# Kernel optimization log

Measured on AMD Instinct MI355X. Metric: run time of the kernel, lower is better.

Reference implementation:

```python
import jax, jax.numpy as jnp
import numpy as np

D_MODEL = 1024
NUM_HEADS = 8
D_HEAD = D_MODEL // NUM_HEADS
EPS = 1e-5


def layer_norm(x, gamma, beta):
    mu = jnp.mean(x, axis=-1, keepdims=True)
    var = jnp.mean((x - mu) ** 2, axis=-1, keepdims=True)
    return (x - mu) * jax.lax.rsqrt(var + EPS) * gamma + beta


def setup_inputs() -> dict:
    key = jax.random.key(0)
    ks = jax.random.split(key, 16)
    B, N, M, D = 4, 1024, 1024, D_MODEL
    s = 0.02
    inp = {
        "input_states": jax.random.normal(ks[0], (B, N, D), jnp.float32),
        "memory_states": jax.random.normal(ks[1], (B, M, D), jnp.float32),
        "memory_weights": jax.random.uniform(ks[2], (B, M), jnp.float32),
        "memory_masks": jax.random.randint(ks[3], (B, M), 0, 2).astype(bool),
        "attention_factors": jax.random.uniform(ks[4], (B, N, M), jnp.float32),
        "attention_masks": jax.random.randint(ks[5], (B, 1, N, M), 0, 2).astype(bool),
        "Wq": jax.random.normal(ks[6], (D, D), jnp.float32) * s,
        "bq": jnp.zeros((D,), jnp.float32),
        "Wk": jax.random.normal(ks[7], (D, D), jnp.float32) * s,
        "bk": jnp.zeros((D,), jnp.float32),
        "Wv": jax.random.normal(ks[8], (D, D), jnp.float32) * s,
        "bv": jnp.zeros((D,), jnp.float32),
        "Wo": jax.random.normal(ks[9], (D, D), jnp.float32) * s,
        "bo": jnp.zeros((D,), jnp.float32),
        "g1": jnp.ones((D,), jnp.float32),
        "b1": jnp.zeros((D,), jnp.float32),
        "We": jax.random.normal(ks[10], (2 * D, D), jnp.float32) * s,
        "be": jnp.zeros((2 * D,), jnp.float32),
        "Ws": jax.random.normal(ks[11], (D, 2 * D), jnp.float32) * s,
        "bs": jnp.zeros((D,), jnp.float32),
        "g2": jnp.ones((D,), jnp.float32),
        "b2": jnp.zeros((D,), jnp.float32),
    }
    return inp


def reference(input_states, memory_states, memory_weights, memory_masks,
              attention_factors, attention_masks,
              Wq, bq, Wk, bk, Wv, bv, Wo, bo, g1, b1,
              We, be, Ws, bs, g2, b2):
    B, N, D = input_states.shape
    M = memory_states.shape[1]
    H, C = NUM_HEADS, D_HEAD
    # QKV projections, split heads: (B, H, len, C)
    q = (input_states @ Wq.T + bq).reshape(B, N, H, C).transpose(0, 2, 1, 3)
    k = (memory_states @ Wk.T + bk).reshape(B, M, H, C).transpose(0, 2, 1, 3)
    v = (memory_states @ Wv.T + bv).reshape(B, M, H, C).transpose(0, 2, 1, 3)
    scores = jnp.einsum('bhnc,bhmc->bhnm', q, k) / jnp.sqrt(jnp.float32(C))
    scores = attention_factors[:, None, :, :] * scores
    scores = scores * memory_weights[:, None, None, :]
    neg_inf = jnp.float32(-jnp.inf)
    scores = jnp.where(memory_masks[:, None, None, :], neg_inf, scores)
    scores = jnp.where(attention_masks, neg_inf, scores)
    attn = jax.nn.softmax(scores, axis=-1)  # (B,H,N,M)
    hidden = jnp.einsum('bhnm,bhmc->bhnc', attn, v)
    hidden = hidden.transpose(0, 2, 1, 3).reshape(B, N, D)
    hidden = hidden @ Wo.T + bo
    out1 = layer_norm(hidden + input_states, g1, b1)
    # FFN: expand -> ReLU -> squeeze -> residual + LN
    h = jax.nn.relu(out1 @ We.T + be)
    h = h @ Ws.T + bs
    out = layer_norm(out1 + h, g2, b2)
    return out, attn
```

## Files before the change

### kernel.cpp

```cpp
#include <hip/hip_runtime.h>
#include <hip/hip_bf16.h>

typedef __bf16 bf16_t;
typedef __bf16 bf16x4 __attribute__((ext_vector_type(4)));
typedef __bf16 bf16x8 __attribute__((ext_vector_type(8)));
typedef float f32x4 __attribute__((ext_vector_type(4)));

typedef const __attribute__((address_space(1))) void gvoid_t;
typedef __attribute__((address_space(3))) void lvoid_t;

#define MB (1UL<<20)
#define NEGINF (-__builtin_inff())
#define SCALE 0.08838834764831845f

__device__ __forceinline__ void gload_lds16(const void* g, void* l) {
    __builtin_amdgcn_global_load_lds((gvoid_t*)g, (lvoid_t*)l, 16, 0, 0);
}

__global__ __launch_bounds__(256) void cast_kernel(const float* __restrict__ in,
                                                   bf16_t* __restrict__ out, int n4) {
    int i = blockIdx.x * 256 + threadIdx.x;
    if (i < n4) {
        float4 f = ((const float4*)in)[i];
        bf16x4 o;
        o[0] = (bf16_t)f.x; o[1] = (bf16_t)f.y; o[2] = (bf16_t)f.z; o[3] = (bf16_t)f.w;
        ((bf16x4*)out)[i] = o;
    }
}

template<int TM, int OUT_BF16, int HAS_BIAS, int RELU, int HAS_RES, int VT_OUT>
__global__ __launch_bounds__(256)
void gemm_bt(const bf16_t* __restrict__ Ap, int lda,
             const bf16_t* __restrict__ Bp, int ldb,
             const float* __restrict__ bias,
             const float* __restrict__ res, int ldres,
             void* __restrict__ Cp, int ldc,
             int K, int tilesN,
             long aOffB, long aOffH, long bOffB, long bOffH, long cOffZ, int nH)
{
    __shared__ bf16_t sA[2 * TM * 32];
    __shared__ bf16_t sB[2 * 128 * 32];

    const int z = blockIdx.y;
    const int zb = z / nH, zh = z % nH;
    Ap += zb * aOffB + zh * aOffH;
    Bp += zb * bOffB + zh * bOffH;
    const long cOff = (long)z * cOffZ;

    const int tile = blockIdx.x;
    const int tm = tile / tilesN, tn = tile % tilesN;
    const int rowBase = tm * TM, colBase = tn * 128;
    const int t = threadIdx.x;
    const int wave = t >> 6, lane = t & 63;
    const int wr = (TM == 128) ? ((wave >> 1) * 64) : 0;
    const int wc = (TM == 128) ? ((wave & 1) * 64) : (wave * 32);
    constexpr int NF = (TM == 128) ? 4 : 2;

    f32x4 acc[4][NF] = {};

    const int e0 = t * 8;
    const int srow = e0 >> 5, scol = e0 & 31;

    auto stage = [&](int tt, int bi) {
        const int k0 = tt * 32;
        #pragma unroll
        for (int r = 0; r < TM / 64; ++r) {
            const int row = r * 64 + srow;
            gload_lds16(Ap + (long)(rowBase + row) * lda + k0 + scol,
                        (char*)sA + bi * (TM * 64) + r * 4096 + wave * 1024);
        }
        #pragma unroll
        for (int r = 0; r < 2; ++r) {
            const int row = r * 64 + srow;
            gload_lds16(Bp + (long)(colBase + row) * ldb + k0 + scol,
                        (char*)sB + bi * 8192 + r * 4096 + wave * 1024);
        }
    };

    const int nt = K >> 5;
    stage(0, 0);
    asm volatile("s_waitcnt vmcnt(0)" ::: "memory");
    __syncthreads();

    const int kf = (lane >> 4) * 8;
    const int lr = lane & 15;

    for (int tt = 0; tt < nt; ++tt) {
        const int cur = tt & 1;
        if (tt + 1 < nt) stage(tt + 1, cur ^ 1);

        bf16x8 af[4], bfr[NF];
        #pragma unroll
        for (int m = 0; m < 4; ++m)
            af[m] = *(const bf16x8*)&sA[cur * (TM * 32) + (wr + m * 16 + lr) * 32 + kf];
        #pragma unroll
        for (int n = 0; n < NF; ++n)
            bfr[n] = *(const bf16x8*)&sB[cur * 4096 + (wc + n * 16 + lr) * 32 + kf];
        #pragma unroll
        for (int m = 0; m < 4; ++m)
            #pragma unroll
            for (int n = 0; n < NF; ++n)
                acc[m][n] = __builtin_amdgcn_mfma_f32_16x16x32_bf16(af[m], bfr[n], acc[m][n], 0, 0, 0);

        asm volatile("s_waitcnt vmcnt(0)" ::: "memory");
        __syncthreads();
    }

    #pragma unroll
    for (int m = 0; m < 4; ++m) {
        #pragma unroll
        for (int r = 0; r < 4; ++r) {
            const int i = rowBase + wr + m * 16 + (lane >> 4) * 4 + r;
            #pragma unroll
            for (int n = 0; n < NF; ++n) {
                const int j = colBase + wc + n * 16 + (lane & 15);
                float v = acc[m][n][r];
                if constexpr (HAS_BIAS) v += bias[j];
                if constexpr (RELU) v = fmaxf(v, 0.0f);
                if constexpr (HAS_RES) v += res[(long)i * ldres + j];
                if constexpr (VT_OUT) {
                    const long o = (((long)(i >> 10) * 8 + (j >> 7)) * 128 + (j & 127)) * 1024 + (i & 1023);
                    ((bf16_t*)Cp)[o] = (bf16_t)v;
                } else if constexpr (OUT_BF16) {
                    ((bf16_t*)Cp)[cOff + (long)i * ldc + j] = (bf16_t)v;
                } else {
                    ((float*)Cp)[cOff + (long)i * ldc + j] = v;
                }
            }
        }
    }
}

__global__ __launch_bounds__(256)
void gate_stats_kernel(float* __restrict__ Sio,
                       const float* __restrict__ factors,
                       const float* __restrict__ weights,
                       const int* __restrict__ mmask,
                       const int* __restrict__ amask,
                       float2* __restrict__ stats)
{
    const int row = blockIdx.x * 4 + (threadIdx.x >> 6);
    const int lane = threadIdx.x & 63;
    const int n = row & 1023;
    const int b = row >> 13;
    float4* p = (float4*)(Sio + (long)row * 1024);
    const float4* fac = (const float4*)(factors + ((long)b * 1024 + n) * 1024);
    const float4* wt  = (const float4*)(weights + (long)b * 1024);
    const int4*   mm  = (const int4*)(mmask + (long)b * 1024);
    const int4*   am  = (const int4*)(amask + ((long)b * 1024 + n) * 1024);

    float vals[16];
    float mx = NEGINF;
    #pragma unroll
    for (int jj = 0; jj < 4; ++jj) {
        const int v4 = lane + jj * 64;
        float4 sc = p[v4];
        float4 fa = fac[v4];
        float4 w4 = wt[v4];
        int4 m4 = mm[v4];
        int4 a4 = am[v4];
        float4 g;
        g.x = (m4.x | a4.x) ? NEGINF : sc.x * SCALE * fa.x * w4.x;
        g.y = (m4.y | a4.y) ? NEGINF : sc.y * SCALE * fa.y * w4.y;
        g.z = (m4.z | a4.z) ? NEGINF : sc.z * SCALE * fa.z * w4.z;
        g.w = (m4.w | a4.w) ? NEGINF : sc.w * SCALE * fa.w * w4.w;
        p[v4] = g;
        vals[jj * 4 + 0] = g.x; vals[jj * 4 + 1] = g.y;
        vals[jj * 4 + 2] = g.z; vals[jj * 4 + 3] = g.w;
        mx = fmaxf(mx, fmaxf(fmaxf(g.x, g.y), fmaxf(g.z, g.w)));
    }
    #pragma unroll
    for (int off = 32; off > 0; off >>= 1) mx = fmaxf(mx, __shfl_xor(mx, off));
    float sum = 0.f;
    #pragma unroll
    for (int q = 0; q < 16; ++q) sum += __expf(vals[q] - mx);
    #pragma unroll
    for (int off = 32; off > 0; off >>= 1) sum += __shfl_xor(sum, off);
    if (lane == 0) {
        float2 o; o.x = mx; o.y = 1.0f / sum;
        stats[row] = o;
    }
}

__global__ __launch_bounds__(256)
void pv_kernel(float* __restrict__ Sio,
               const bf16_t* __restrict__ Vtb,
               const float2* __restrict__ stats,
               bf16_t* __restrict__ hidb)
{
    __shared__ bf16_t sA[2 * 64 * 32];
    __shared__ bf16_t sB[2 * 128 * 32];

    const int bh = blockIdx.y;
    const int b = bh >> 3, h = bh & 7;
    const int rowBase = blockIdx.x * 64;
    const int t = threadIdx.x;
    const int wave = t >> 6, lane = t & 63;
    const int wc = wave * 32;

    float* Sp = Sio + (long)bh * 1048576;
    const bf16_t* Bp = Vtb + (long)bh * 131072;

    const int arow = rowBase + (t >> 2);
    const int acol = (t & 3) * 8;
    float* Srow = Sp + (long)arow * 1024 + acol;
    const float2 ML = stats[(long)bh * 1024 + arow];

    f32x4 acc[4][2] = {};

    auto stageB = [&](int tt, int bi) {
        const int k0 = tt * 32;
        #pragma unroll
        for (int r = 0; r < 2; ++r) {
            const int row = r * 64 + ((t * 8) >> 5);
            gload_lds16(Bp + (long)row * 1024 + k0 + ((t * 8) & 31),
                        (char*)sB + bi * 8192 + r * 4096 + wave * 1024);
        }
    };

    auto procA = [&](int tt, int bi, float4 s0, float4 s1) {
        float p[8];
        p[0] = __expf(s0.x - ML.x) * ML.y; p[1] = __expf(s0.y - ML.x) * ML.y;
        p[2] = __expf(s0.z - ML.x) * ML.y; p[3] = __expf(s0.w - ML.x) * ML.y;
        p[4] = __expf(s1.x - ML.x) * ML.y; p[5] = __expf(s1.y - ML.x) * ML.y;
        p[6] = __expf(s1.z - ML.x) * ML.y; p[7] = __expf(s1.w - ML.x) * ML.y;
        float* sp = Srow + tt * 32;
        float4 o0, o1;
        o0.x = p[0]; o0.y = p[1]; o0.z = p[2]; o0.w = p[3];
        o1.x = p[4]; o1.y = p[5]; o1.z = p[6]; o1.w = p[7];
        *(float4*)sp = o0;
        *(float4*)(sp + 4) = o1;
        bf16x8 pb;
        #pragma unroll
        for (int q = 0; q < 8; ++q) pb[q] = (bf16_t)p[q];
        *(bf16x8*)((char*)sA + bi * 4096 + t * 16) = pb;
    };

    stageB(0, 0);
    {
        float4 s0 = *(const float4*)Srow;
        float4 s1 = *(const float4*)(Srow + 4);
        procA(0, 0, s0, s1);
    }
    asm volatile("s_waitcnt vmcnt(0)" ::: "memory");
    __syncthreads();

    const int kf = (lane >> 4) * 8;
    const int lr = lane & 15;

    for (int tt = 0; tt < 32; ++tt) {
        const int cur = tt & 1;
        float4 s0, s1;
        if (tt < 31) {
            stageB(tt + 1, cur ^ 1);
            s0 = *(const float4*)(Srow + (tt + 1) * 32);
            s1 = *(const float4*)(Srow + (tt + 1) * 32 + 4);
        }

        bf16x8 af[4], bfr[2];
        #pragma unroll
        for (int m = 0; m < 4; ++m)
            af[m] = *(const bf16x8*)&sA[cur * 2048 + (m * 16 + lr) * 32 + kf];
        #pragma unroll
        for (int n = 0; n < 2; ++n)
            bfr[n] = *(const bf16x8*)&sB[cur * 4096 + (wc + n * 16 + lr) * 32 + kf];
        #pragma unroll
        for (int m = 0; m < 4; ++m)
            #pragma unroll
            for (int n = 0; n < 2; ++n)
                acc[m][n] = __builtin_amdgcn_mfma_f32_16x16x32_bf16(af[m], bfr[n], acc[m][n], 0, 0, 0);

        if (tt < 31) procA(tt + 1, cur ^ 1, s0, s1);

        asm volatile("s_waitcnt vmcnt(0)" ::: "memory");
        __syncthreads();
    }

    #pragma unroll
    for (int m = 0; m < 4; ++m) {
        #pragma unroll
        for (int r = 0; r < 4; ++r) {
            const int i = rowBase + m * 16 + (lane >> 4) * 4 + r;
            #pragma unroll
            for (int n = 0; n < 2; ++n) {
                const int j = wc + n * 16 + (lane & 15);
                hidb[((long)b * 1024 + i) * 1024 + h * 128 + j] = (bf16_t)acc[m][n][r];
            }
        }
    }
}

template<int WRITE_BF16>
__global__ __launch_bounds__(256)
void ln_kernel(const float* __restrict__ x,
               const float* __restrict__ g,
               const float* __restrict__ bt,
               float* __restrict__ outf,
               bf16_t* __restrict__ outb)
{
    const int row = blockIdx.x * 4 + (threadIdx.x >> 6);
    const int lane = threadIdx.x & 63;
    const float* p = x + (long)row * 1024;
    float v[16];
    float s = 0.f;
    #pragma unroll
    for (int jj = 0; jj < 4; ++jj) {
        float4 f = ((const float4*)p)[lane + jj * 64];
        v[jj * 4 + 0] = f.x; v[jj * 4 + 1] = f.y; v[jj * 4 + 2] = f.z; v[jj * 4 + 3] = f.w;
        s += f.x + f.y + f.z + f.w;
    }
    #pragma unroll
    for (int off = 32; off > 0; off >>= 1) s += __shfl_xor(s, off);
    const float mu = s * (1.0f / 1024.0f);
    float q = 0.f;
    #pragma unroll
    for (int i = 0; i < 16; ++i) { float d = v[i] - mu; q += d * d; }
    #pragma unroll
    for (int off = 32; off > 0; off >>= 1) q += __shfl_xor(q, off);
    const float rstd = rsqrtf(q * (1.0f / 1024.0f) + 1e-5f);
    #pragma unroll
    for (int jj = 0; jj < 4; ++jj) {
        const int v4 = lane + jj * 64;
        float4 gg = ((const float4*)g)[v4];
        float4 bb = ((const float4*)bt)[v4];
        float4 o;
        o.x = (v[jj * 4 + 0] - mu) * rstd * gg.x + bb.x;
        o.y = (v[jj * 4 + 1] - mu) * rstd * gg.y + bb.y;
        o.z = (v[jj * 4 + 2] - mu) * rstd * gg.z + bb.z;
        o.w = (v[jj * 4 + 3] - mu) * rstd * gg.w + bb.w;
        ((float4*)outf)[(long)row * 256 + v4] = o;
        if constexpr (WRITE_BF16) {
            bf16x4 ob;
            ob[0] = (bf16_t)o.x; ob[1] = (bf16_t)o.y; ob[2] = (bf16_t)o.z; ob[3] = (bf16_t)o.w;
            ((bf16x4*)outb)[(long)row * 256 + v4] = ob;
        }
    }
}

extern "C" void kernel_launch(void* const* d_in, const int* in_sizes, int n_in,
                              void* d_out, int out_size, void* d_ws, size_t ws_size,
                              hipStream_t stream)
{
    (void)in_sizes; (void)n_in; (void)out_size; (void)ws_size;
    const float* input_states     = (const float*)d_in[0];
    const float* memory_states    = (const float*)d_in[1];
    const float* memory_weights   = (const float*)d_in[2];
    const int*   memory_masks     = (const int*)d_in[3];
    const float* attention_factors= (const float*)d_in[4];
    const int*   attention_masks  = (const int*)d_in[5];
    const float* Wq = (const float*)d_in[6];
    const float* bq = (const float*)d_in[7];
    const float* Wk = (const float*)d_in[8];
    const float* bk = (const float*)d_in[9];
    const float* Wv = (const float*)d_in[10];
    const float* bv = (const float*)d_in[11];
    const float* Wo = (const float*)d_in[12];
    const float* bo = (const float*)d_in[13];
    const float* g1 = (const float*)d_in[14];
    const float* b1 = (const float*)d_in[15];
    const float* We = (const float*)d_in[16];
    const float* be = (const float*)d_in[17];
    const float* Ws = (const float*)d_in[18];
    const float* bs = (const float*)d_in[19];
    const float* g2 = (const float*)d_in[20];
    const float* b2 = (const float*)d_in[21];

    float* out0 = (float*)d_out;
    float* attn = (float*)d_out + 4L * 1024 * 1024;

    char* ws = (char*)d_ws;
    bf16_t* Wqb  = (bf16_t*)(ws + 0 * MB);
    bf16_t* Wkb  = (bf16_t*)(ws + 2 * MB);
    bf16_t* Wvb  = (bf16_t*)(ws + 4 * MB);
    bf16_t* Wob  = (bf16_t*)(ws + 6 * MB);
    bf16_t* Web  = (bf16_t*)(ws + 8 * MB);
    bf16_t* Wsb  = (bf16_t*)(ws + 12 * MB);
    bf16_t* inb  = (bf16_t*)(ws + 16 * MB);
    bf16_t* memb = (bf16_t*)(ws + 24 * MB);
    bf16_t* Qb   = (bf16_t*)(ws + 32 * MB);
    bf16_t* Kb   = (bf16_t*)(ws + 40 * MB);
    bf16_t* Vtb  = (bf16_t*)(ws + 48 * MB);
    bf16_t* hidb = (bf16_t*)(ws + 56 * MB);
    float*  preLN= (float*)(ws + 64 * MB);
    float*  out1f= (float*)(ws + 80 * MB);
    bf16_t* out1b= (bf16_t*)(ws + 96 * MB);
    bf16_t* hffn = (bf16_t*)(ws + 104 * MB);
    float2* stats= (float2*)(ws + 112 * MB);

    auto cast = [&](const float* src, bf16_t* dst, long n) {
        cast_kernel<<<(int)(n / 4 / 256), 256, 0, stream>>>(src, dst, (int)(n / 4));
    };
    cast(Wq, Wqb, 1024L * 1024);
    cast(Wk, Wkb, 1024L * 1024);
    cast(Wv, Wvb, 1024L * 1024);
    cast(Wo, Wob, 1024L * 1024);
    cast(We, Web, 2048L * 1024);
    cast(Ws, Wsb, 1024L * 2048);
    cast(input_states, inb, 4096L * 1024);
    cast(memory_states, memb, 4096L * 1024);

    gemm_bt<64,1,1,0,0,0><<<dim3(512, 1), 256, 0, stream>>>(
        inb, 1024, Wqb, 1024, bq, nullptr, 0, Qb, 1024, 1024, 8, 0,0,0,0,0, 1);
    gemm_bt<64,1,1,0,0,0><<<dim3(512, 1), 256, 0, stream>>>(
        memb, 1024, Wkb, 1024, bk, nullptr, 0, Kb, 1024, 1024, 8, 0,0,0,0,0, 1);
    gemm_bt<64,1,1,0,0,1><<<dim3(512, 1), 256, 0, stream>>>(
        memb, 1024, Wvb, 1024, bv, nullptr, 0, Vtb, 1024, 1024, 8, 0,0,0,0,0, 1);
    gemm_bt<128,0,0,0,0,0><<<dim3(64, 32), 256, 0, stream>>>(
        Qb, 1024, Kb, 1024, nullptr, nullptr, 0, attn, 1024, 128, 8,
        1048576L, 128L, 1048576L, 128L, 1048576L, 8);
    gate_stats_kernel<<<8192, 256, 0, stream>>>(attn, attention_factors,
                                                memory_weights, memory_masks,
                                                attention_masks, stats);
    pv_kernel<<<dim3(16, 32), 256, 0, stream>>>(attn, Vtb, stats, hidb);
    gemm_bt<64,0,1,0,1,0><<<dim3(512, 1), 256, 0, stream>>>(
        hidb, 1024, Wob, 1024, bo, input_states, 1024, preLN, 1024, 1024, 8, 0,0,0,0,0, 1);
    ln_kernel<1><<<1024, 256, 0, stream>>>(preLN, g1, b1, out1f, out1b);
    gemm_bt<64,1,1,1,0,0><<<dim3(1024, 1), 256, 0, stream>>>(
        out1b, 1024, Web, 1024, be, nullptr, 0, hffn, 2048, 1024, 16, 0,0,0,0,0, 1);
    gemm_bt<64,0,1,0,1,0><<<dim3(512, 1), 256, 0, stream>>>(
        hffn, 2048, Wsb, 2048, bs, out1f, 1024, preLN, 1024, 2048, 8, 0,0,0,0,0, 1);
    ln_kernel<0><<<1024, 256, 0, stream>>>(preLN, g2, b2, out0, nullptr);
}
```

Baseline: 376.1 us.

## Finalize softmax in gate kernel and fuse weight/input casts into one launch

The gate kernel now computes normalized softmax probabilities and writes them directly into the attention output, removing the stats buffer. The PV kernel then only reads the probabilities and converts them to bf16, so it no longer recomputes exp or writes the attention matrix a second time. This removes one full read-modify-write pass over the large score tensor. The eight separate fp32-to-bf16 cast launches are merged into a single kernel that selects its source by index range, cutting launch overhead.

```diff
diff --git a/kernel.cpp b/kernel.cpp
--- a/kernel.cpp
+++ b/kernel.cpp
@@ -17,15 +17,30 @@
     __builtin_amdgcn_global_load_lds((gvoid_t*)g, (lvoid_t*)l, 16, 0, 0);
 }
 
-__global__ __launch_bounds__(256) void cast_kernel(const float* __restrict__ in,
-                                                   bf16_t* __restrict__ out, int n4) {
-    int i = blockIdx.x * 256 + threadIdx.x;
-    if (i < n4) {
-        float4 f = ((const float4*)in)[i];
-        bf16x4 o;
-        o[0] = (bf16_t)f.x; o[1] = (bf16_t)f.y; o[2] = (bf16_t)f.z; o[3] = (bf16_t)f.w;
-        ((bf16x4*)out)[i] = o;
-    }
+__global__ __launch_bounds__(256)
+void cast8_kernel(const float* __restrict__ s0, bf16_t* __restrict__ d0,
+                  const float* __restrict__ s1, bf16_t* __restrict__ d1,
+                  const float* __restrict__ s2, bf16_t* __restrict__ d2,
+                  const float* __restrict__ s3, bf16_t* __restrict__ d3,
+                  const float* __restrict__ s4, bf16_t* __restrict__ d4,
+                  const float* __restrict__ s5, bf16_t* __restrict__ d5,
+                  const float* __restrict__ s6, bf16_t* __restrict__ d6,
+                  const float* __restrict__ s7, bf16_t* __restrict__ d7)
+{
+    long i = (long)blockIdx.x * 256 + threadIdx.x;
+    const float* src; bf16_t* dst; long l;
+    if      (i < 262144L)  { src = s0; dst = d0; l = i; }
+    else if (i < 524288L)  { src = s1; dst = d1; l = i - 262144L; }
+    else if (i < 786432L)  { src = s2; dst = d2; l = i - 524288L; }
+    else if (i < 1048576L) { src = s3; dst = d3; l = i - 786432L; }
+    else if (i < 1572864L) { src = s4; dst = d4; l = i - 1048576L; }
+    else if (i < 2097152L) { src = s5; dst = d5; l = i - 1572864L; }
+    else if (i < 3145728L) { src = s6; dst = d6; l = i - 2097152L; }
+    else                   { src = s7; dst = d7; l = i - 3145728L; }
+    float4 f = ((const float4*)src)[l];
+    bf16x4 o;
+    o[0] = (bf16_t)f.x; o[1] = (bf16_t)f.y; o[2] = (bf16_t)f.z; o[3] = (bf16_t)f.w;
+    ((bf16x4*)dst)[l] = o;
 }
 
 template<int TM, int OUT_BF16, int HAS_BIAS, int RELU, int HAS_RES, int VT_OUT>
@@ -132,12 +147,11 @@
 }
 
 __global__ __launch_bounds__(256)
-void gate_stats_kernel(float* __restrict__ Sio,
-                       const float* __restrict__ factors,
-                       const float* __restrict__ weights,
-                       const int* __restrict__ mmask,
-                       const int* __restrict__ amask,
-                       float2* __restrict__ stats)
+void gate_softmax_kernel(float* __restrict__ Sio,
+                         const float* __restrict__ factors,
+                         const float* __restrict__ weights,
+                         const int* __restrict__ mmask,
+                         const int* __restrict__ amask)
 {
     const int row = blockIdx.x * 4 + (threadIdx.x >> 6);
     const int lane = threadIdx.x & 63;
@@ -164,7 +178,6 @@
         g.y = (m4.y | a4.y) ? NEGINF : sc.y * SCALE * fa.y * w4.y;
         g.z = (m4.z | a4.z) ? NEGINF : sc.z * SCALE * fa.z * w4.z;
         g.w = (m4.w | a4.w) ? NEGINF : sc.w * SCALE * fa.w * w4.w;
-        p[v4] = g;
         vals[jj * 4 + 0] = g.x; vals[jj * 4 + 1] = g.y;
         vals[jj * 4 + 2] = g.z; vals[jj * 4 + 3] = g.w;
         mx = fmaxf(mx, fmaxf(fmaxf(g.x, g.y), fmaxf(g.z, g.w)));
@@ -173,19 +186,23 @@
     for (int off = 32; off > 0; off >>= 1) mx = fmaxf(mx, __shfl_xor(mx, off));
     float sum = 0.f;
     #pragma unroll
-    for (int q = 0; q < 16; ++q) sum += __expf(vals[q] - mx);
+    for (int q = 0; q < 16; ++q) { float e = __expf(vals[q] - mx); vals[q] = e; sum += e; }
     #pragma unroll
     for (int off = 32; off > 0; off >>= 1) sum += __shfl_xor(sum, off);
-    if (lane == 0) {
-        float2 o; o.x = mx; o.y = 1.0f / sum;
-        stats[row] = o;
+    const float inv = 1.0f / sum;
+    #pragma unroll
+    for (int jj = 0; jj < 4; ++jj) {
+        const int v4 = lane + jj * 64;
+        float4 o;
+        o.x = vals[jj * 4 + 0] * inv; o.y = vals[jj * 4 + 1] * inv;
+        o.z = vals[jj * 4 + 2] * inv; o.w = vals[jj * 4 + 3] * inv;
+        p[v4] = o;
     }
 }
 
 __global__ __launch_bounds__(256)
-void pv_kernel(float* __restrict__ Sio,
+void pv_kernel(const float* __restrict__ Sprob,
                const bf16_t* __restrict__ Vtb,
-               const float2* __restrict__ stats,
                bf16_t* __restrict__ hidb)
 {
     __shared__ bf16_t sA[2 * 64 * 32];
@@ -198,13 +215,12 @@
     const int wave = t >> 6, lane = t & 63;
     const int wc = wave * 32;
 
-    float* Sp = Sio + (long)bh * 1048576;
+    const float* Sp = Sprob + (long)bh * 1048576;
     const bf16_t* Bp = Vtb + (long)bh * 131072;
 
     const int arow = rowBase + (t >> 2);
     const int acol = (t & 3) * 8;
-    float* Srow = Sp + (long)arow * 1024 + acol;
-    const float2 ML = stats[(long)bh * 1024 + arow];
+    const float* Srow = Sp + (long)arow * 1024 + acol;
 
     f32x4 acc[4][2] = {};
 
@@ -219,20 +235,9 @@
     };
 
     auto procA = [&](int tt, int bi, float4 s0, float4 s1) {
-        float p[8];
-        p[0] = __expf(s0.x - ML.x) * ML.y; p[1] = __expf(s0.y - ML.x) * ML.y;
-        p[2] = __expf(s0.z - ML.x) * ML.y; p[3] = __expf(s0.w - ML.x) * ML.y;
-        p[4] = __expf(s1.x - ML.x) * ML.y; p[5] = __expf(s1.y - ML.x) * ML.y;
-        p[6] = __expf(s1.z - ML.x) * ML.y; p[7] = __expf(s1.w - ML.x) * ML.y;
-        float* sp = Srow + tt * 32;
-        float4 o0, o1;
-        o0.x = p[0]; o0.y = p[1]; o0.z = p[2]; o0.w = p[3];
-        o1.x = p[4]; o1.y = p[5]; o1.z = p[6]; o1.w = p[7];
-        *(float4*)sp = o0;
-        *(float4*)(sp + 4) = o1;
         bf16x8 pb;
-        #pragma unroll
-        for (int q = 0; q < 8; ++q) pb[q] = (bf16_t)p[q];
+        pb[0] = (bf16_t)s0.x; pb[1] = (bf16_t)s0.y; pb[2] = (bf16_t)s0.z; pb[3] = (bf16_t)s0.w;
+        pb[4] = (bf16_t)s1.x; pb[5] = (bf16_t)s1.y; pb[6] = (bf16_t)s1.z; pb[7] = (bf16_t)s1.w;
         *(bf16x8*)((char*)sA + bi * 4096 + t * 16) = pb;
     };
 
@@ -385,19 +390,10 @@
     float*  out1f= (float*)(ws + 80 * MB);
     bf16_t* out1b= (bf16_t*)(ws + 96 * MB);
     bf16_t* hffn = (bf16_t*)(ws + 104 * MB);
-    float2* stats= (float2*)(ws + 112 * MB);
-
-    auto cast = [&](const float* src, bf16_t* dst, long n) {
-        cast_kernel<<<(int)(n / 4 / 256), 256, 0, stream>>>(src, dst, (int)(n / 4));
-    };
-    cast(Wq, Wqb, 1024L * 1024);
-    cast(Wk, Wkb, 1024L * 1024);
-    cast(Wv, Wvb, 1024L * 1024);
-    cast(Wo, Wob, 1024L * 1024);
-    cast(We, Web, 2048L * 1024);
-    cast(Ws, Wsb, 1024L * 2048);
-    cast(input_states, inb, 4096L * 1024);
-    cast(memory_states, memb, 4096L * 1024);
+
+    cast8_kernel<<<16384, 256, 0, stream>>>(Wq, Wqb, Wk, Wkb, Wv, Wvb, Wo, Wob,
+                                            We, Web, Ws, Wsb,
+                                            input_states, inb, memory_states, memb);
 
     gemm_bt<64,1,1,0,0,0><<<dim3(512, 1), 256, 0, stream>>>(
         inb, 1024, Wqb, 1024, bq, nullptr, 0, Qb, 1024, 1024, 8, 0,0,0,0,0, 1);
@@ -408,10 +404,10 @@
     gemm_bt<128,0,0,0,0,0><<<dim3(64, 32), 256, 0, stream>>>(
         Qb, 1024, Kb, 1024, nullptr, nullptr, 0, attn, 1024, 128, 8,
         1048576L, 128L, 1048576L, 128L, 1048576L, 8);
-    gate_stats_kernel<<<8192, 256, 0, stream>>>(attn, attention_factors,
-                                                memory_weights, memory_masks,
-                                                attention_masks, stats);
-    pv_kernel<<<dim3(16, 32), 256, 0, stream>>>(attn, Vtb, stats, hidb);
+    gate_softmax_kernel<<<8192, 256, 0, stream>>>(attn, attention_factors,
+                                                  memory_weights, memory_masks,
+                                                  attention_masks);
+    pv_kernel<<<dim3(16, 32), 256, 0, stream>>>(attn, Vtb, hidb);
     gemm_bt<64,0,1,0,1,0><<<dim3(512, 1), 256, 0, stream>>>(
         hidb, 1024, Wob, 1024, bo, input_states, 1024, preLN, 1024, 1024, 8, 0,0,0,0,0, 1);
     ln_kernel<1><<<1024, 256, 0, stream>>>(preLN, g1, b1, out1f, out1b);
```

Result: faster. 337.2 us (-10.4%).
